# Performance work log

Measured on AMD Instinct MI355X. Metric: run time of the kernel, lower is better.

The kernel has to match this reference:

```python
import jax, jax.numpy as jnp
import numpy as np

B, C, H, W, L, R = 1, 32, 96, 128, 2, 3
N = 2 * R + 1
EPS = 1e-5


def conv2d(x, w, stride=1, pad=1):
    return jax.lax.conv_general_dilated(
        x, w, (stride, stride), ((pad, pad), (pad, pad)),
        dimension_numbers=('NCHW', 'OIHW', 'NCHW'))


def conv_transpose2d(x, w, stride=2, pad=1):
    # torch ConvTranspose2d semantics; w: [Cin, Cout, kH, kW]
    kh, kw = w.shape[2], w.shape[3]
    wf = jnp.flip(w, (2, 3)).transpose(1, 0, 2, 3)  # [Cout, Cin, kh, kw]
    return jax.lax.conv_general_dilated(
        x, wf, (1, 1),
        ((kh - 1 - pad, kh - 1 - pad), (kw - 1 - pad, kw - 1 - pad)),
        lhs_dilation=(stride, stride),
        dimension_numbers=('NCHW', 'OIHW', 'NCHW'))


def bnorm(x, s, b, m, v):
    # inference-mode BatchNorm2d (fixed running stats)
    inv = s * jax.lax.rsqrt(v + EPS)
    return x * inv[None, :, None, None] + (b - m * inv)[None, :, None, None]


def grid_sample(img, grid):
    # bilinear, align_corners=True, padding_mode='zeros'
    # img [B,C,H,W], grid [B,Hg,Wg,2] (x,y) in [-1,1]
    Bi, Ci, Hi, Wi = img.shape
    gx = (grid[..., 0] + 1.0) * 0.5 * (Wi - 1)
    gy = (grid[..., 1] + 1.0) * 0.5 * (Hi - 1)
    x0 = jnp.floor(gx)
    y0 = jnp.floor(gy)
    wx = (gx - x0)[:, None]  # [B,1,Hg,Wg]
    wy = (gy - y0)[:, None]

    def tap(yf, xf):
        valid = (xf >= 0) & (xf <= Wi - 1) & (yf >= 0) & (yf <= Hi - 1)
        xc = jnp.clip(xf, 0, Wi - 1).astype(jnp.int32)
        yc = jnp.clip(yf, 0, Hi - 1).astype(jnp.int32)
        v = jax.vmap(lambda im, y, x: im[:, y, x])(img, yc, xc)  # [B,C,Hg,Wg]
        return v * valid[:, None].astype(img.dtype)

    v00 = tap(y0, x0)
    v01 = tap(y0, x0 + 1)
    v10 = tap(y0 + 1, x0)
    v11 = tap(y0 + 1, x0 + 1)
    return (v00 * (1 - wx) * (1 - wy) + v01 * wx * (1 - wy)
            + v10 * (1 - wx) * wy + v11 * wx * wy)


def _forward(fmap1_0, fmap1_1, fmap2_0, fmap2_1, coords,
             cw1, cw2, cw3, cw4, ctw5, cw6, cb6,
             bn1s, bn1b, bn1m, bn1v, bn2s, bn2b, bn2m, bn2v,
             bn3s, bn3b, bn3m, bn3v, bn4s, bn4b, bn4m, bn4v,
             bn5s, bn5b, bn5m, bn5v, dap_w):
    n = N
    dx = jnp.linspace(-R, R, n)
    delta = jnp.stack(jnp.meshgrid(dx, dx, indexing='ij'), axis=-1)  # [n,n,2]
    b, _, h, w = coords.shape
    cp = coords.transpose(0, 2, 3, 1)  # [b,h,w,2] (x,y)
    bns = ((bn1s, bn1b, bn1m, bn1v), (bn2s, bn2b, bn2m, bn2v),
           (bn3s, bn3b, bn3m, bn3v), (bn4s, bn4b, bn4m, bn4v),
           (bn5s, bn5b, bn5m, bn5v))
    out = []
    for i, (f1, f2) in enumerate(((fmap1_0, fmap2_0), (fmap1_1, fmap2_1))):
        c, h2, w2 = f1.shape[1], f1.shape[2], f1.shape[3]
        # [b,n,h,n,w,2]: first n axis pairs with h, second with w (as in torch view)
        cent = cp[:, None, :, None, :, :] / (2.0 ** i) + delta[None, :, None, :, None, :]
        gx = 2.0 * cent[..., 0] / (w2 - 1) - 1.0
        gy = 2.0 * cent[..., 1] / (h2 - 1) - 1.0
        grid = jnp.stack([gx, gy], -1).reshape(b, n * h, n * w, 2)
        f2s = grid_sample(f2, grid).reshape(b, c, n, h, n, w)
        f2s = f2s.transpose(0, 2, 4, 1, 3, 5)  # [b,du,dv,c,h,w]
        f1e = jnp.broadcast_to(f1[:, None, None], (b, n, n, c, h, w))
        x = jnp.concatenate([f1e, f2s], axis=3).reshape(b * n * n, 2 * c, h, w)
        # MatchingNet (DICL): conv-bn-relu stack, stride-2 down + transposed up
        x = jax.nn.relu(bnorm(conv2d(x, cw1[i]), *(p[i] for p in bns[0])))
        x = jax.nn.relu(bnorm(conv2d(x, cw2[i], stride=2), *(p[i] for p in bns[1])))
        x = jax.nn.relu(bnorm(conv2d(x, cw3[i]), *(p[i] for p in bns[2])))
        x = jax.nn.relu(bnorm(conv2d(x, cw4[i]), *(p[i] for p in bns[3])))
        x = jax.nn.relu(bnorm(conv_transpose2d(x, ctw5[i]), *(p[i] for p in bns[4])))
        x = conv2d(x, cw6[i]) + cb6[i][None, :, None, None]  # [b*n*n,1,h,w]
        cost = x.reshape(b, n * n, h, w)
        # DisplacementAwareProjection: 1x1 conv over the 49 displacement channels
        cost = jnp.einsum('pq,bqhw->bphw', dap_w[i], cost)
        out.append(cost)
    return jnp.concatenate(out, axis=1)  # [b, L*(2r+1)^2, h, w]


def setup_inputs():
    key = jax.random.key(0)
    ks = jax.random.split(key, 40)

    def rn(k, shape, scale=1.0):
        return jax.random.normal(k, shape, jnp.float32) * scale

    inp = {}
    inp['fmap1_0'] = rn(ks[0], (B, C, H, W))
    inp['fmap2_0'] = rn(ks[1], (B, C, H, W))
    inp['fmap1_1'] = rn(ks[2], (B, C, H, W))
    inp['fmap2_1'] = rn(ks[3], (B, C, H, W))
    gy, gx = jnp.meshgrid(jnp.arange(H, dtype=jnp.float32),
                          jnp.arange(W, dtype=jnp.float32), indexing='ij')
    base = jnp.stack([gx, gy], 0)[None]  # [1,2,H,W] (x,y) pixel coords
    inp['coords'] = base + rn(ks[4], (B, 2, H, W), 2.0)

    def cw(k, co, ci, kk):
        return rn(k, (L, co, ci, kk, kk), 1.0 / np.sqrt(ci * kk * kk))

    inp['cw1'] = cw(ks[5], 96, 2 * C, 3)
    inp['cw2'] = cw(ks[6], 128, 96, 3)
    inp['cw3'] = cw(ks[7], 128, 128, 3)
    inp['cw4'] = cw(ks[8], 64, 128, 3)
    inp['ctw5'] = rn(ks[9], (L, 64, 32, 4, 4), 1.0 / np.sqrt(64 * 16))
    inp['cw6'] = cw(ks[10], 1, 32, 3)
    inp['cb6'] = rn(ks[11], (L, 1), 0.1)
    for j, ch in enumerate((96, 128, 128, 64, 32), start=1):
        k4 = jax.random.split(ks[11 + j], 4)
        inp['bn%ds' % j] = 1.0 + rn(k4[0], (L, ch), 0.1)
        inp['bn%db' % j] = rn(k4[1], (L, ch), 0.1)
        inp['bn%dm' % j] = rn(k4[2], (L, ch), 0.1)
        inp['bn%dv' % j] = 1.0 + rn(k4[3], (L, ch), 0.1) ** 2
    # DAP identity init
    inp['dap_w'] = jnp.tile(jnp.eye(N * N, dtype=jnp.float32)[None], (L, 1, 1))
    return inp


def reference(fmap1_0, fmap1_1, fmap2_0, fmap2_1, coords,
              cw1, cw2, cw3, cw4, ctw5, cw6, cb6,
              bn1s, bn1b, bn1m, bn1v, bn2s, bn2b, bn2m, bn2v,
              bn3s, bn3b, bn3m, bn3v, bn4s, bn4b, bn4m, bn4v,
              bn5s, bn5b, bn5m, bn5v, dap_w):
    return _forward(fmap1_0, fmap1_1, fmap2_0, fmap2_1, coords,
                    cw1, cw2, cw3, cw4, ctw5, cw6, cb6,
                    bn1s, bn1b, bn1m, bn1v, bn2s, bn2b, bn2m, bn2v,
                    bn3s, bn3b, bn3m, bn3v, bn4s, bn4b, bn4m, bn4v,
                    bn5s, bn5b, bn5m, bn5v, dap_w)
```

## Files before the change

kernel.cpp:

```cpp
#include <hip/hip_runtime.h>

#define EPSF 1e-5f

typedef __attribute__((ext_vector_type(8))) short short8;
typedef __attribute__((ext_vector_type(4))) float f32x4;

__device__ __forceinline__ ushort f2bf(float x) {
    union { float f; unsigned u; } c; c.f = x;
    unsigned r = c.u + 0x7FFF + ((c.u >> 16) & 1);
    return (ushort)(r >> 16);
}
__device__ __forceinline__ float bf2f(ushort b) {
    union { unsigned u; float f; } c; c.u = ((unsigned)b) << 16;
    return c.f;
}
__device__ __forceinline__ int swz(int a) {
    return a ^ (((a >> 7) & 7) << 4);
}


__global__ __launch_bounds__(256) void k_repack_conv(
    const float* __restrict__ src, ushort* __restrict__ dst, int CO, int CI)
{
    int idx = blockIdx.x * 256 + threadIdx.x;
    if (idx >= CO * CI * 9) return;
    int co = idx / (CI * 9);
    int rem = idx % (CI * 9);
    int ci = rem / 9, tap = rem % 9;
    dst[((size_t)tap * CO + co) * CI + ci] = f2bf(src[idx]);
}

__global__ __launch_bounds__(256) void k_repack_ct(
    const float* __restrict__ src, ushort* __restrict__ dst)
{
    int idx = blockIdx.x * 256 + threadIdx.x;
    if (idx >= 4 * 4 * 32 * 64) return;
    int ci = idx & 63;
    int t = idx >> 6;
    int co = t & 31; t >>= 5;
    int tap = t & 3;
    int parity = t >> 2;
    int ph = parity >> 1, pw = parity & 1;
    int a = tap >> 1, b = tap & 1;
    int kh = ((ph + 1) & 1) + 2 * a;
    int kw = ((pw + 1) & 1) + 2 * b;
    dst[idx] = f2bf(src[((ci * 32 + co) * 4 + kh) * 4 + kw]);
}

__global__ __launch_bounds__(256) void k_pack_f1(
    const float* __restrict__ f1_0, const float* __restrict__ f1_1,
    ushort* __restrict__ xf1)
{
    const int sp = blockIdx.x * 256 + threadIdx.x;
    const int l = blockIdx.z;
    const float* f1 = l ? f1_1 : f1_0;
    ushort* dst = xf1 + (size_t)l * 393216 + (size_t)sp * 32;
    #pragma unroll
    for (int g = 0; g < 4; ++g) {
        uint4 pk;
        uint* pw_ = (uint*)&pk;
        #pragma unroll
        for (int q = 0; q < 4; ++q) {
            int c = g * 8 + q * 2;
            pw_[q] = (uint)f2bf(f1[(size_t)c * 12288 + sp])
                   | ((uint)f2bf(f1[(size_t)(c + 1) * 12288 + sp]) << 16);
        }
        *(uint4*)(dst + g * 8) = pk;
    }
}

__global__ __launch_bounds__(256) void k_sample_nhwc(
    const float* __restrict__ f2_0, const float* __restrict__ f2_1,
    const float* __restrict__ coords, ushort* __restrict__ x0s, int d0)
{
    const int HW = 12288;
    const int sp = blockIdx.x * 256 + threadIdx.x;
    const int slot = blockIdx.z;
    const int p = d0 + slot;
    const int l = p / 49;
    const int d = p - l * 49;
    const int du = d / 7, dv = d % 7;
    const float inv_scale = l ? 0.5f : 1.0f;
    const float* f2 = l ? f2_1 : f2_0;

    float cx = coords[sp] * inv_scale + (float)(du - 3);
    float cy = coords[HW + sp] * inv_scale + (float)(dv - 3);
    float xf = floorf(cx), yf = floorf(cy);
    float wx = cx - xf, wy = cy - yf;
    int xi = (int)xf, yi = (int)yf;
    float vx0 = (xf >= 0.f && xf <= 127.f) ? 1.f : 0.f;
    float vx1 = (xf + 1.f >= 0.f && xf + 1.f <= 127.f) ? 1.f : 0.f;
    float vy0 = (yf >= 0.f && yf <= 95.f) ? 1.f : 0.f;
    float vy1 = (yf + 1.f >= 0.f && yf + 1.f <= 95.f) ? 1.f : 0.f;
    int x0i = min(max(xi, 0), 127), x1i = min(max(xi + 1, 0), 127);
    int y0i = min(max(yi, 0), 95),  y1i = min(max(yi + 1, 0), 95);
    float w00 = (1.f - wx) * (1.f - wy) * vx0 * vy0;
    float w01 = wx * (1.f - wy) * vx1 * vy0;
    float w10 = (1.f - wx) * wy * vx0 * vy1;
    float w11 = wx * wy * vx1 * vy1;
    int o00 = y0i * 128 + x0i, o01 = y0i * 128 + x1i;
    int o10 = y1i * 128 + x0i, o11 = y1i * 128 + x1i;

    ushort* dst = x0s + ((size_t)slot * HW + sp) * 32;
    #pragma unroll
    for (int g = 0; g < 4; ++g) {
        uint4 pk;
        uint* pw_ = (uint*)&pk;
        #pragma unroll
        for (int q = 0; q < 4; ++q) {
            uint wv = 0;
            #pragma unroll
            for (int h = 0; h < 2; ++h) {
                int c = g * 8 + q * 2 + h;
                const float* fc = f2 + (size_t)c * HW;
                float s = w00 * fc[o00] + w01 * fc[o01] + w10 * fc[o10] + w11 * fc[o11];
                wv |= ((uint)f2bf(s)) << (16 * h);
            }
            pw_[q] = wv;
        }
        *(uint4*)(dst + g * 8) = pk;
    }
}

template <int EPI>
__global__ __launch_bounds__(512, 2) void k_conv1(
    const ushort* __restrict__ in,
    ushort* __restrict__ out,
    const ushort* __restrict__ wbase,
    const float* __restrict__ p1,
    const float* __restrict__ bs0, const float* __restrict__ bb0,
    const float* __restrict__ bm0, const float* __restrict__ bv0,
    int d0, int koff)
{
    constexpr int AB = 10 * 66 * 64;
    constexpr int PB = 3 * 48 * 64;
    constexpr int SA = 6;
    __shared__ __align__(16) char smem[AB + 2 * PB];
    char* As = smem;

    const int tid = threadIdx.x;
    const int lane = tid & 63, wid = tid >> 6;
    const int lr = lane & 15, kg = lane >> 4;
    const int bx = blockIdx.x;
    const int rt = bx >> 1, ct = bx & 1;
    const int r0 = rt * 8, c0 = ct * 64;
    const int y = blockIdx.y;
    const int co0 = y * 48;
    const int slot = blockIdx.z;
    const int l = EPI ? slot : (d0 + slot) / 49;

    const ushort* ib = in + (size_t)slot * 12288 * 32;
    const ushort* wl = wbase + (size_t)l * (9 * 96 * 64);
    const short8 z8 = {0, 0, 0, 0, 0, 0, 0, 0};

    #pragma unroll
    for (int i = 0; i < SA; ++i) {
        int lin = i * 8192 + tid * 16;
        if (lin < AB) {
            int pos = lin >> 6;
            int prow = (pos * 994) >> 16;
            int pcol = pos - prow * 66;
            int grow = r0 - 1 + prow, gcol = c0 - 1 + pcol;
            bool ok = ((unsigned)grow < 96u) && ((unsigned)gcol < 128u);
            short8 v = z8;
            if (ok) v = *(const short8*)(ib + (grow * 128 + gcol) * 32 + ((lin & 63) >> 1));
            *(short8*)(As + swz(lin)) = v;
        }
    }

    int boff[2]; unsigned bmask = 0;
    #pragma unroll
    for (int i = 0; i < 2; ++i) {
        int lin = i * 8192 + tid * 16;
        if (lin < PB) bmask |= 1u << i;
        int lc = min(lin, PB - 16);
        int rowidx = lc >> 6;
        int tpg = rowidx / 48;
        int r = rowidx - tpg * 48;
        boff[i] = (tpg * 96 + co0 + r) * 64 + koff + ((lc & 63) >> 1);
    }
    short8 stgB[2];
    auto loadB = [&](int pg) {
        const ushort* src = wl + pg * (3 * 96 * 64);
        #pragma unroll
        for (int i = 0; i < 2; ++i)
            if ((bmask >> i) & 1) stgB[i] = *(const short8*)(src + boff[i]);
    };
    auto writeB = [&](int pg) {
        char* Bs = smem + AB + (pg & 1) * PB;
        #pragma unroll
        for (int i = 0; i < 2; ++i) {
            int lin = i * 8192 + tid * 16;
            if ((bmask >> i) & 1) *(short8*)(Bs + swz(lin)) = stgB[i];
        }
    };

    f32x4 acc[4][3];
    if constexpr (EPI == 0) {
        const float* pl = p1 + (size_t)l * 1179648
                        + ((size_t)((bx * 2 + y) * 512 + tid)) * 48;
        #pragma unroll
        for (int mf = 0; mf < 4; ++mf)
            #pragma unroll
            for (int nf = 0; nf < 3; ++nf)
                acc[mf][nf] = *(const f32x4*)(pl + (mf * 3 + nf) * 4);
    } else {
        #pragma unroll
        for (int mf = 0; mf < 4; ++mf)
            #pragma unroll
            for (int nf = 0; nf < 3; ++nf)
                acc[mf][nf] = (f32x4){0.f, 0.f, 0.f, 0.f};
    }

    loadB(0);
    writeB(0);
    __syncthreads();

    #pragma unroll
    for (int ps = 0; ps < 3; ++ps) {
        if (ps < 2) loadB(ps + 1);
        const char* Bs = smem + AB + (ps & 1) * PB;
        #pragma unroll
        for (int kw = 0; kw < 3; ++kw) {
            short8 a[4];
            #pragma unroll
            for (int mf = 0; mf < 4; ++mf) {
                int sp = (wid + ps) * 66 + mf * 16 + lr + kw;
                a[mf] = *(const short8*)(As + swz(sp * 64 + kg * 16));
            }
            #pragma unroll
            for (int nf = 0; nf < 3; ++nf) {
                short8 b = *(const short8*)(Bs + swz((kw * 48 + nf * 16 + lr) * 64 + kg * 16));
                #pragma unroll
                for (int mf = 0; mf < 4; ++mf)
                    acc[mf][nf] = __builtin_amdgcn_mfma_f32_16x16x32_bf16(
                        a[mf], b, acc[mf][nf], 0, 0, 0);
            }
        }
        __syncthreads();
        if (ps < 2) { writeB(ps + 1); __syncthreads(); }
    }

    if constexpr (EPI == 1) {
        float* of = (float*)out + (size_t)l * 1179648
                  + ((size_t)((bx * 2 + y) * 512 + tid)) * 48;
        #pragma unroll
        for (int mf = 0; mf < 4; ++mf)
            #pragma unroll
            for (int nf = 0; nf < 3; ++nf)
                *(f32x4*)(of + (mf * 3 + nf) * 4) = acc[mf][nf];
    } else {
        const float* bs = bs0 + l * 96;
        const float* bb = bb0 + l * 96;
        const float* bm = bm0 + l * 96;
        const float* bv = bv0 + l * 96;
        ushort* ob = out + (size_t)slot * 12288 * 96;
        const int orow = r0 + wid;
        #pragma unroll
        for (int nf = 0; nf < 3; ++nf) {
            const int col = co0 + nf * 16 + lr;
            const float inv = bs[col] * rsqrtf(bv[col] + EPSF);
            const float beta = bb[col] - bm[col] * inv;
            #pragma unroll
            for (int mf = 0; mf < 4; ++mf) {
                #pragma unroll
                for (int j = 0; j < 4; ++j) {
                    int ocol = c0 + mf * 16 + kg * 4 + j;
                    float yv = fmaxf(fmaf(acc[mf][nf][j], inv, beta), 0.f);
                    ob[((size_t)orow * 128 + ocol) * 96 + col] = f2bf(yv);
                }
            }
        }
    }
}

template <int CIN, int COUT, int IH, int IW>
__global__ __launch_bounds__(512, 4) void k_conv_lds8s(
    const ushort* __restrict__ in, ushort* __restrict__ out,
    const ushort* __restrict__ wbase, int wlstride,
    const float* __restrict__ bs0, const float* __restrict__ bb0,
    const float* __restrict__ bm0, const float* __restrict__ bv0, int d0)
{
    constexpr int CCs = CIN / 32;
    constexpr int AB = 10 * 66 * 64;
    constexpr int PB = 3 * 64 * 64;
    constexpr int SA = 6, SB = 2;
    constexpr int NPH = 3 * CCs;
    __shared__ __align__(16) char smem[AB + 2 * PB];
    char* As = smem;

    const int tid = threadIdx.x;
    const int lane = tid & 63, wid = tid >> 6;
    const int lr = lane & 15, kg = lane >> 4;
    const int r0 = (int)blockIdx.x * 8;
    const int co0 = (int)blockIdx.y * 64;
    const int slot = blockIdx.z;
    const int l = (d0 + slot) / 49;

    int aoff[SA]; unsigned awr = 0, avalid = 0;
    #pragma unroll
    for (int i = 0; i < SA; ++i) {
        int lin = i * 8192 + tid * 16;
        bool wr = lin < AB;
        int linc = wr ? lin : 0;
        int pos = linc >> 6;
        int prow = (pos * 994) >> 16;
        int pcol = pos - prow * 66;
        int grow = r0 - 1 + prow, gcol = pcol - 1;
        bool ok = wr && ((unsigned)grow < (unsigned)IH) && ((unsigned)gcol < (unsigned)IW);
        if (wr) awr |= 1u << i;
        if (ok) avalid |= 1u << i;
        int growc = min(max(grow, 0), IH - 1), gcolc = min(max(gcol, 0), IW - 1);
        aoff[i] = (growc * IW + gcolc) * CIN + ((linc & 63) >> 1);
    }
    int boff[SB]; unsigned bmask = 0;
    #pragma unroll
    for (int i = 0; i < SB; ++i) {
        int lin = i * 8192 + tid * 16;
        if (lin < PB) bmask |= 1u << i;
        int lc = min(lin, PB - 16);
        int rowidx = lc >> 6;
        int tpg = rowidx >> 6, r = rowidx & 63;
        boff[i] = (tpg * COUT + co0 + r) * CIN + ((lc & 63) >> 1);
    }

    const ushort* ib = in + (size_t)slot * IH * IW * CIN;
    const ushort* wl = wbase + (size_t)l * wlstride;
    const short8 z8 = {0, 0, 0, 0, 0, 0, 0, 0};

    auto stageA = [&](int cc) {
        #pragma unroll
        for (int i = 0; i < SA; ++i) {
            int lin = i * 8192 + tid * 16;
            if ((awr >> i) & 1) {
                short8 v = z8;
                if ((avalid >> i) & 1)
                    v = *(const short8*)(ib + aoff[i] + cc * 32);
                *(short8*)(As + swz(lin)) = v;
            }
        }
    };
    short8 stgB[SB];
    auto loadB = [&](int ps) {
        int pg = ps % 3, cc = ps / 3;
        const ushort* src = wl + pg * (3 * COUT * CIN) + cc * 32;
        #pragma unroll
        for (int i = 0; i < SB; ++i)
            if ((bmask >> i) & 1) stgB[i] = *(const short8*)(src + boff[i]);
    };
    auto writeB = [&](int ps) {
        char* Bs = smem + AB + (ps & 1) * PB;
        #pragma unroll
        for (int i = 0; i < SB; ++i) {
            int lin = i * 8192 + tid * 16;
            if ((bmask >> i) & 1) *(short8*)(Bs + swz(lin)) = stgB[i];
        }
    };

    f32x4 acc[4][4];
    #pragma unroll
    for (int mf = 0; mf < 4; ++mf)
        #pragma unroll
        for (int nf = 0; nf < 4; ++nf)
            acc[mf][nf] = (f32x4){0.f, 0.f, 0.f, 0.f};

    stageA(0);
    loadB(0); writeB(0);
    __syncthreads();

    #pragma unroll 1
    for (int ps = 0; ps < NPH; ++ps) {
        const int pg = ps % 3;
        const bool hasNext = (ps + 1 < NPH);
        if (hasNext) loadB(ps + 1);

        const char* Bs = smem + AB + (ps & 1) * PB;
        #pragma unroll
        for (int kw = 0; kw < 3; ++kw) {
            short8 a[4];
            #pragma unroll
            for (int mf = 0; mf < 4; ++mf) {
                int sp = (wid + pg) * 66 + mf * 16 + lr + kw;
                a[mf] = *(const short8*)(As + swz(sp * 64 + kg * 16));
            }
            #pragma unroll
            for (int nf = 0; nf < 4; ++nf) {
                short8 b = *(const short8*)(Bs + swz((kw * 64 + nf * 16 + lr) * 64 + kg * 16));
                #pragma unroll
                for (int mf = 0; mf < 4; ++mf)
                    acc[mf][nf] = __builtin_amdgcn_mfma_f32_16x16x32_bf16(
                        a[mf], b, acc[mf][nf], 0, 0, 0);
            }
        }

        __syncthreads();
        if (hasNext) {
            writeB(ps + 1);
            if (pg == 2) stageA(ps / 3 + 1);
            __syncthreads();
        }
    }

    const float* bs = bs0 + l * COUT;
    const float* bb = bb0 + l * COUT;
    const float* bm = bm0 + l * COUT;
    const float* bv = bv0 + l * COUT;
    ushort* ob = out + (size_t)slot * IH * IW * COUT;
    const int orow = r0 + wid;
    #pragma unroll
    for (int nf = 0; nf < 4; ++nf) {
        const int col = co0 + nf * 16 + lr;
        const float inv = bs[col] * rsqrtf(bv[col] + EPSF);
        const float beta = bb[col] - bm[col] * inv;
        #pragma unroll
        for (int mf = 0; mf < 4; ++mf) {
            #pragma unroll
            for (int j = 0; j < 4; ++j) {
                int ocol = mf * 16 + kg * 4 + j;
                float y = fmaxf(fmaf(acc[mf][nf][j], inv, beta), 0.f);
                ob[((size_t)orow * IW + ocol) * COUT + col] = f2bf(y);
            }
        }
    }
}

__global__ __launch_bounds__(512, 2) void k_conv_s2_8(
    const ushort* __restrict__ in, ushort* __restrict__ out,
    const ushort* __restrict__ wbase, int wlstride,
    const float* __restrict__ bs0, const float* __restrict__ bb0,
    const float* __restrict__ bm0, const float* __restrict__ bv0, int d0)
{
    constexpr int AB = 9 * 66 * 64;
    constexpr int PB = 3 * 64 * 64;
    constexpr int SA = 5;
    constexpr int SB = 2;
    constexpr int NPH = 9;
    __shared__ __align__(16) char smem[AB + 2 * PB];
    char* As = smem;

    const int tid = threadIdx.x;
    const int lane = tid & 63, wid = tid >> 6;
    const int lr = lane & 15, kg = lane >> 4;
    const int mw = wid >> 1, ch = wid & 1;
    const int bx = blockIdx.x;
    const int rt = bx >> 1, ct = bx & 1;
    const int r0 = rt * 4, oc0 = ct * 32;
    const int co0 = blockIdx.y * 64;
    const int slot = blockIdx.z;
    const int l = (d0 + slot) / 49;

    int aoff[SA]; unsigned awr = 0, avalid = 0;
    #pragma unroll
    for (int i = 0; i < SA; ++i) {
        int lin = i * 8192 + tid * 16;
        bool wr = lin < AB;
        int linc = wr ? lin : 0;
        int pos = linc >> 6;
        int prow = (pos * 994) >> 16;
        int pcol = pos - prow * 66;
        int grow = 2 * r0 - 1 + prow, gcol = 2 * oc0 - 1 + pcol;
        bool ok = wr && ((unsigned)grow < 96u) && ((unsigned)gcol < 128u);
        if (wr) awr |= 1u << i;
        if (ok) avalid |= 1u << i;
        int growc = min(max(grow, 0), 95), gcolc = min(max(gcol, 0), 127);
        aoff[i] = (growc * 128 + gcolc) * 96 + ((linc & 63) >> 1);
    }
    int boff[SB]; unsigned bmask = 0;
    #pragma unroll
    for (int i = 0; i < SB; ++i) {
        int lin = i * 8192 + tid * 16;
        if (lin < PB) bmask |= 1u << i;
        int lc = min(lin, PB - 16);
        int rowidx = lc >> 6;
        int tpg = rowidx >> 6, r = rowidx & 63;
        boff[i] = (tpg * 128 + co0 + r) * 96 + ((lc & 63) >> 1);
    }

    const ushort* ib = in + (size_t)slot * 12288 * 96;
    const ushort* wl = wbase + (size_t)l * wlstride;
    const short8 z8 = {0, 0, 0, 0, 0, 0, 0, 0};

    short8 stgA[SA], stgB[SB];
    auto loadA = [&](int cc) {
        #pragma unroll
        for (int i = 0; i < SA; ++i) {
            if ((avalid >> i) & 1) stgA[i] = *(const short8*)(ib + aoff[i] + cc * 32);
            else stgA[i] = z8;
        }
    };
    auto writeA = [&]() {
        #pragma unroll
        for (int i = 0; i < SA; ++i) {
            int lin = i * 8192 + tid * 16;
            if ((awr >> i) & 1)
                *(short8*)(As + swz(lin)) = stgA[i];
        }
    };
    auto loadB = [&](int ps) {
        int pg = ps % 3, cc = ps / 3;
        const ushort* src = wl + pg * (3 * 128 * 96) + cc * 32;
        #pragma unroll
        for (int i = 0; i < SB; ++i)
            if ((bmask >> i) & 1) stgB[i] = *(const short8*)(src + boff[i]);
    };
    auto writeB = [&](int ps) {
        char* Bs = smem + AB + (ps & 1) * PB;
        #pragma unroll
        for (int i = 0; i < SB; ++i) {
            int lin = i * 8192 + tid * 16;
            if ((bmask >> i) & 1)
                *(short8*)(Bs + swz(lin)) = stgB[i];
        }
    };

    f32x4 acc[2][2];
    #pragma unroll
    for (int mf = 0; mf < 2; ++mf)
        #pragma unroll
        for (int nf = 0; nf < 2; ++nf)
            acc[mf][nf] = (f32x4){0.f, 0.f, 0.f, 0.f};

    loadA(0); loadB(0);
    writeA(); writeB(0);
    __syncthreads();

    #pragma unroll 1
    for (int ps = 0; ps < NPH; ++ps) {
        const int pg = ps % 3;
        const bool hasNext = (ps + 1 < NPH);
        const bool newA = (pg == 2) && hasNext;
        if (hasNext) loadB(ps + 1);
        if (newA) loadA(ps / 3 + 1);

        const char* Bs = smem + AB + (ps & 1) * PB;
        #pragma unroll
        for (int kw = 0; kw < 3; ++kw) {
            short8 a[2];
            #pragma unroll
            for (int mf = 0; mf < 2; ++mf) {
                int pos = (2 * mw + pg) * 66 + 2 * (mf * 16 + lr) + kw;
                a[mf] = *(const short8*)(As + swz(pos * 64 + kg * 16));
            }
            #pragma unroll
            for (int nf = 0; nf < 2; ++nf) {
                int rb = kw * 64 + ch * 32 + nf * 16 + lr;
                short8 b = *(const short8*)(Bs + swz(rb * 64 + kg * 16));
                #pragma unroll
                for (int mf = 0; mf < 2; ++mf)
                    acc[mf][nf] = __builtin_amdgcn_mfma_f32_16x16x32_bf16(
                        a[mf], b, acc[mf][nf], 0, 0, 0);
            }
        }

        __syncthreads();
        if (hasNext) writeB(ps + 1);
        if (newA) writeA();
        if (hasNext) __syncthreads();
    }

    const float* bs = bs0 + l * 128;
    const float* bb = bb0 + l * 128;
    const float* bm = bm0 + l * 128;
    const float* bv = bv0 + l * 128;
    ushort* ob = out + (size_t)slot * 3072 * 128;
    const int orow = r0 + mw;
    #pragma unroll
    for (int nf = 0; nf < 2; ++nf) {
        const int col = co0 + ch * 32 + nf * 16 + lr;
        const float inv = bs[col] * rsqrtf(bv[col] + EPSF);
        const float beta = bb[col] - bm[col] * inv;
        #pragma unroll
        for (int mf = 0; mf < 2; ++mf) {
            #pragma unroll
            for (int j = 0; j < 4; ++j) {
                int ocol = oc0 + mf * 16 + kg * 4 + j;
                float y = fmaxf(fmaf(acc[mf][nf][j], inv, beta), 0.f);
                ob[((size_t)orow * 64 + ocol) * 128 + col] = f2bf(y);
            }
        }
    }
}

__global__ __launch_bounds__(512, 4) void k_convt_lds(
    const ushort* __restrict__ in, ushort* __restrict__ out,
    const ushort* __restrict__ wbase,
    const float* __restrict__ bs0, const float* __restrict__ bb0,
    const float* __restrict__ bm0, const float* __restrict__ bv0, int d0)
{
    constexpr int AB = 10 * 66 * 64;
    constexpr int PB = 4 * 32 * 64;
    constexpr int SA = 6;
    __shared__ __align__(16) char smem[AB + 2 * PB];
    char* As = smem;

    const int tid = threadIdx.x;
    const int lane = tid & 63, wid = tid >> 6;
    const int lr = lane & 15, kg = lane >> 4;
    const int q0 = (int)blockIdx.x * 8;
    const int parity = blockIdx.y;
    const int ph = parity >> 1, pw = parity & 1;
    const int slot = blockIdx.z;
    const int l = (d0 + slot) / 49;

    int aoff[SA]; unsigned awr = 0, avalid = 0;
    #pragma unroll
    for (int i = 0; i < SA; ++i) {
        int lin = i * 8192 + tid * 16;
        bool wr = lin < AB;
        int linc = wr ? lin : 0;
        int pos = linc >> 6;
        int prow = (pos * 994) >> 16;
        int pcol = pos - prow * 66;
        int grow = q0 - 1 + prow, gcol = pcol - 1;
        bool ok = wr && ((unsigned)grow < 48u) && ((unsigned)gcol < 64u);
        if (wr) awr |= 1u << i;
        if (ok) avalid |= 1u << i;
        int growc = min(max(grow, 0), 47), gcolc = min(max(gcol, 0), 63);
        aoff[i] = (growc * 64 + gcolc) * 64 + ((linc & 63) >> 1);
    }
    int boffB;
    {
        int lin = tid * 16;
        int rowidx = lin >> 6;
        int tap = rowidx >> 5, co = rowidx & 31;
        boffB = ((parity * 4 + tap) * 32 + co) * 64 + ((lin & 63) >> 1);
    }

    const ushort* ib = in + (size_t)slot * 3072 * 64;
    const ushort* wl = wbase + (size_t)l * (16 * 32 * 64);
    const short8 z8 = {0, 0, 0, 0, 0, 0, 0, 0};

    auto stageA = [&](int cc) {
        #pragma unroll
        for (int i = 0; i < SA; ++i) {
            int lin = i * 8192 + tid * 16;
            if ((awr >> i) & 1) {
                short8 v = z8;
                if ((avalid >> i) & 1)
                    v = *(const short8*)(ib + aoff[i] + cc * 32);
                *(short8*)(As + swz(lin)) = v;
            }
        }
    };
    short8 stgB;
    auto loadB = [&](int cc) {
        stgB = *(const short8*)(wl + boffB + cc * 32);
    };
    auto writeB = [&](int cc) {
        char* Bs = smem + AB + (cc & 1) * PB;
        *(short8*)(Bs + swz(tid * 16)) = stgB;
    };

    f32x4 acc[4][2];
    #pragma unroll
    for (int mf = 0; mf < 4; ++mf)
        #pragma unroll
        for (int nf = 0; nf < 2; ++nf)
            acc[mf][nf] = (f32x4){0.f, 0.f, 0.f, 0.f};

    stageA(0);
    loadB(0); writeB(0);
    __syncthreads();

    #pragma unroll 1
    for (int cc = 0; cc < 2; ++cc) {
        if (cc == 0) loadB(1);
        const char* Bs = smem + AB + (cc & 1) * PB;
        #pragma unroll
        for (int a = 0; a < 2; ++a) {
            #pragma unroll
            for (int b2 = 0; b2 < 2; ++b2) {
                const int tap = a * 2 + b2;
                short8 av[4];
                #pragma unroll
                for (int mf = 0; mf < 4; ++mf) {
                    int pos = (wid + 1 + ph - a) * 66 + mf * 16 + lr + pw - b2 + 1;
                    av[mf] = *(const short8*)(As + swz(pos * 64 + kg * 16));
                }
                #pragma unroll
                for (int nf = 0; nf < 2; ++nf) {
                    short8 b = *(const short8*)(Bs
                        + swz((tap * 32 + nf * 16 + lr) * 64 + kg * 16));
                    #pragma unroll
                    for (int mf = 0; mf < 4; ++mf)
                        acc[mf][nf] = __builtin_amdgcn_mfma_f32_16x16x32_bf16(
                            av[mf], b, acc[mf][nf], 0, 0, 0);
                }
            }
        }
        __syncthreads();
        if (cc == 0) {
            writeB(1);
            stageA(1);
            __syncthreads();
        }
    }

    const float* bs = bs0 + l * 32;
    const float* bb = bb0 + l * 32;
    const float* bm = bm0 + l * 32;
    const float* bv = bv0 + l * 32;
    ushort* ob = out + (size_t)slot * 12288 * 32;
    const size_t rowb = (size_t)(2 * (q0 + wid) + ph) * 128;
    #pragma unroll
    for (int nf = 0; nf < 2; ++nf) {
        const int col = nf * 16 + lr;
        const float inv = bs[col] * rsqrtf(bv[col] + EPSF);
        const float beta = bb[col] - bm[col] * inv;
        #pragma unroll
        for (int mf = 0; mf < 4; ++mf) {
            #pragma unroll
            for (int j = 0; j < 4; ++j) {
                int r = mf * 16 + kg * 4 + j;
                float y = fmaxf(fmaf(acc[mf][nf][j], inv, beta), 0.f);
                ob[(rowb + 2 * r + pw) * 32 + col] = f2bf(y);
            }
        }
    }
}

__global__ __launch_bounds__(256) void k_conv6(
    const ushort* __restrict__ x5, float* __restrict__ cost,
    const float* __restrict__ w0, const float* __restrict__ cb6, int d0)
{
    const int sp = blockIdx.x * 256 + threadIdx.x;
    const int slot = blockIdx.z;
    const int p = d0 + slot;
    const int l = p / 49;
    const float* w = w0 + l * 288;
    const int oh = sp >> 7, ow = sp & 127;
    float acc = 0.f;
    #pragma unroll
    for (int kh = 0; kh < 3; ++kh) {
        const int ih = oh - 1 + kh;
        if (ih < 0 || ih >= 96) continue;
        #pragma unroll
        for (int kw = 0; kw < 3; ++kw) {
            const int iw = ow - 1 + kw;
            if (iw < 0 || iw >= 128) continue;
            const ushort* q = x5 + ((size_t)slot * 12288 + ih * 128 + iw) * 32;
            const int tap = kh * 3 + kw;
            #pragma unroll
            for (int g = 0; g < 4; ++g) {
                uint4 v = *(const uint4*)(q + g * 8);
                const uint* vw = (const uint*)&v;
                #pragma unroll
                for (int t = 0; t < 4; ++t) {
                    int ci = g * 8 + t * 2;
                    acc = fmaf(bf2f((ushort)(vw[t] & 0xFFFF)), w[ci * 9 + tap], acc);
                    acc = fmaf(bf2f((ushort)(vw[t] >> 16)), w[(ci + 1) * 9 + tap], acc);
                }
            }
        }
    }
    cost[(size_t)p * 12288 + sp] = acc + cb6[l];
}

__global__ __launch_bounds__(256) void k_dap(
    const float* __restrict__ cost, const float* __restrict__ dw,
    float* __restrict__ out)
{
    const int sp = blockIdx.x * 256 + threadIdx.x;
    const int p = blockIdx.y;
    const float* dr = dw + p * 49;
    float acc = 0.f;
    #pragma unroll
    for (int q = 0; q < 49; ++q)
        acc = fmaf(dr[q], cost[(size_t)q * 12288 + sp], acc);
    out[(size_t)p * 12288 + sp] = acc;
}

extern "C" void kernel_launch(void* const* d_in, const int* in_sizes, int n_in,
                              void* d_out, int out_size, void* d_ws, size_t ws_size,
                              hipStream_t stream)
{
    const float* fm1_0 = (const float*)d_in[0];
    const float* fm2_0 = (const float*)d_in[1];
    const float* fm1_1 = (const float*)d_in[2];
    const float* fm2_1 = (const float*)d_in[3];
    const float* coords = (const float*)d_in[4];
    const float* cw1  = (const float*)d_in[5];
    const float* cw2  = (const float*)d_in[6];
    const float* cw3  = (const float*)d_in[7];
    const float* cw4  = (const float*)d_in[8];
    const float* ctw5 = (const float*)d_in[9];
    const float* cw6  = (const float*)d_in[10];
    const float* cb6  = (const float*)d_in[11];
    const float* bn[5][4];
    for (int j = 0; j < 5; ++j)
        for (int k = 0; k < 4; ++k)
            bn[j][k] = (const float*)d_in[12 + j * 4 + k];
    const float* dap = (const float*)d_in[32];
    float* out = (float*)d_out;

    const size_t A_US = 393216;
    const size_t B_US = 1179648;
    const size_t XF1 = 2 * 393216;
    const size_t W1 = 9 * 96 * 64, W2 = 9 * 128 * 96, W3 = 9 * 128 * 128;
    const size_t W4 = 9 * 64 * 128, W5 = 16 * 32 * 64;
    const size_t W_US = 2 * (W1 + W2 + W3 + W4 + W5);
    const size_t P1F = 2 * (size_t)24 * 2 * 512 * 48;
    const size_t COSTF = (size_t)98 * 12288;

    int DC = 1;
    for (int cand : {98, 66, 49, 42, 33, 25, 17, 13, 9, 7, 5, 3, 2, 1}) {
        size_t need = (A_US + B_US) * (size_t)cand * 2 + (XF1 + W_US) * 2
                    + (P1F + COSTF) * 4 + 4096;
        if (need <= ws_size) { DC = cand; break; }
    }

    ushort* bufA = (ushort*)d_ws;
    ushort* bufB = bufA + A_US * DC;
    ushort* xf1 = bufB + B_US * DC;
    ushort* wp = xf1 + XF1;
    ushort* wr1 = wp; wp += 2 * W1;
    ushort* wr2 = wp; wp += 2 * W2;
    ushort* wr3 = wp; wp += 2 * W3;
    ushort* wr4 = wp; wp += 2 * W4;
    ushort* wr5 = wp; wp += 2 * W5;
    float* P1 = (float*)wp;
    float* cost = P1 + P1F;

    for (int l = 0; l < 2; ++l) {
        k_repack_conv<<<dim3(216), 256, 0, stream>>>(cw1 + (size_t)l * W1, wr1 + l * W1, 96, 64);
        k_repack_conv<<<dim3(432), 256, 0, stream>>>(cw2 + (size_t)l * W2, wr2 + l * W2, 128, 96);
        k_repack_conv<<<dim3(576), 256, 0, stream>>>(cw3 + (size_t)l * W3, wr3 + l * W3, 128, 128);
        k_repack_conv<<<dim3(288), 256, 0, stream>>>(cw4 + (size_t)l * W4, wr4 + l * W4, 64, 128);
        k_repack_ct<<<dim3(128), 256, 0, stream>>>(ctw5 + (size_t)l * W5, wr5 + l * W5);
    }

    k_pack_f1<<<dim3(48, 1, 2), 256, 0, stream>>>(fm1_0, fm1_1, xf1);
    k_conv1<1><<<dim3(24, 2, 2), 512, 0, stream>>>(
        xf1, (ushort*)P1, wr1, nullptr,
        bn[0][0], bn[0][1], bn[0][2], bn[0][3], 0, 0);

    for (int d0 = 0; d0 < 98; d0 += DC) {
        const int ndd = min(DC, 98 - d0);
        k_sample_nhwc<<<dim3(48, 1, ndd), 256, 0, stream>>>(
            fm2_0, fm2_1, coords, bufA, d0);
        k_conv1<0><<<dim3(24, 2, ndd), 512, 0, stream>>>(
            bufA, bufB, wr1, P1,
            bn[0][0], bn[0][1], bn[0][2], bn[0][3], d0, 32);
        k_conv_s2_8<<<dim3(24, 2, ndd), 512, 0, stream>>>(bufB, bufA, wr2, (int)W2,
                bn[1][0], bn[1][1], bn[1][2], bn[1][3], d0);
        k_conv_lds8s<128, 128, 48, 64>
            <<<dim3(6, 2, ndd), 512, 0, stream>>>(bufA, bufB, wr3, (int)W3,
                bn[2][0], bn[2][1], bn[2][2], bn[2][3], d0);
        k_conv_lds8s<128, 64, 48, 64>
            <<<dim3(6, 1, ndd), 512, 0, stream>>>(bufB, bufA, wr4, (int)W4,
                bn[3][0], bn[3][1], bn[3][2], bn[3][3], d0);
        k_convt_lds<<<dim3(6, 4, ndd), 512, 0, stream>>>(bufA, bufB, wr5,
                bn[4][0], bn[4][1], bn[4][2], bn[4][3], d0);
        k_conv6<<<dim3(48, 1, ndd), 256, 0, stream>>>(
            bufB, cost, cw6, cb6, d0);
    }
    for (int l = 0; l < 2; ++l)
        k_dap<<<dim3(48, 49), 256, 0, stream>>>(
            cost + (size_t)l * 49 * 12288, dap + (size_t)l * 49 * 49,
            out + (size_t)l * 49 * 12288);
}
```

Baseline: 735.8 us.

## Compute all 128 output channels per block in stride-2 conv, single-buffer weights

```diff
diff --git a/kernel.cpp b/kernel.cpp
--- a/kernel.cpp
+++ b/kernel.cpp
@@ -424,28 +424,28 @@
     }
 }
 
-__global__ __launch_bounds__(512, 2) void k_conv_s2_8(
+__global__ __launch_bounds__(512, 4) void k_conv_s2_8(
     const ushort* __restrict__ in, ushort* __restrict__ out,
     const ushort* __restrict__ wbase, int wlstride,
     const float* __restrict__ bs0, const float* __restrict__ bb0,
     const float* __restrict__ bm0, const float* __restrict__ bv0, int d0)
 {
     constexpr int AB = 9 * 66 * 64;
-    constexpr int PB = 3 * 64 * 64;
+    constexpr int PB = 3 * 128 * 64;
     constexpr int SA = 5;
-    constexpr int SB = 2;
+    constexpr int SB = 3;
     constexpr int NPH = 9;
-    __shared__ __align__(16) char smem[AB + 2 * PB];
+    __shared__ __align__(16) char smem[AB + PB];
     char* As = smem;
 
     const int tid = threadIdx.x;
     const int lane = tid & 63, wid = tid >> 6;
     const int lr = lane & 15, kg = lane >> 4;
-    const int mw = wid >> 1, ch = wid & 1;
+    const int mw = wid >> 2;
+    const int cw = wid & 3;
     const int bx = blockIdx.x;
     const int rt = bx >> 1, ct = bx & 1;
     const int r0 = rt * 4, oc0 = ct * 32;
-    const int co0 = blockIdx.y * 64;
     const int slot = blockIdx.z;
     const int l = (d0 + slot) / 49;
 
@@ -465,97 +465,92 @@
         int growc = min(max(grow, 0), 95), gcolc = min(max(gcol, 0), 127);
         aoff[i] = (growc * 128 + gcolc) * 96 + ((linc & 63) >> 1);
     }
-    int boff[SB]; unsigned bmask = 0;
+    int boff[SB];
     #pragma unroll
     for (int i = 0; i < SB; ++i) {
         int lin = i * 8192 + tid * 16;
-        if (lin < PB) bmask |= 1u << i;
-        int lc = min(lin, PB - 16);
-        int rowidx = lc >> 6;
-        int tpg = rowidx >> 6, r = rowidx & 63;
-        boff[i] = (tpg * 128 + co0 + r) * 96 + ((lc & 63) >> 1);
+        int rowidx = lin >> 6;
+        int tpg = rowidx >> 7, r = rowidx & 127;
+        boff[i] = (tpg * 128 + r) * 96 + ((lin & 63) >> 1);
     }
 
     const ushort* ib = in + (size_t)slot * 12288 * 96;
     const ushort* wl = wbase + (size_t)l * wlstride;
     const short8 z8 = {0, 0, 0, 0, 0, 0, 0, 0};
 
-    short8 stgA[SA], stgB[SB];
-    auto loadA = [&](int cc) {
-        #pragma unroll
-        for (int i = 0; i < SA; ++i) {
-            if ((avalid >> i) & 1) stgA[i] = *(const short8*)(ib + aoff[i] + cc * 32);
-            else stgA[i] = z8;
-        }
-    };
-    auto writeA = [&]() {
+    auto stageA = [&](int cc) {
         #pragma unroll
         for (int i = 0; i < SA; ++i) {
             int lin = i * 8192 + tid * 16;
-            if ((awr >> i) & 1)
-                *(short8*)(As + swz(lin)) = stgA[i];
-        }
-    };
+            if ((awr >> i) & 1) {
+                short8 v = z8;
+                if ((avalid >> i) & 1)
+                    v = *(const short8*)(ib + aoff[i] + cc * 32);
+                *(short8*)(As + swz(lin)) = v;
+            }
+        }
+    };
+    short8 stgB[SB];
     auto loadB = [&](int ps) {
         int pg = ps % 3, cc = ps / 3;
         const ushort* src = wl + pg * (3 * 128 * 96) + cc * 32;
         #pragma unroll
         for (int i = 0; i < SB; ++i)
-            if ((bmask >> i) & 1) stgB[i] = *(const short8*)(src + boff[i]);
-    };
-    auto writeB = [&](int ps) {
-        char* Bs = smem + AB + (ps & 1) * PB;
+            stgB[i] = *(const short8*)(src + boff[i]);
+    };
+    auto writeB = [&]() {
+        char* Bs = smem + AB;
         #pragma unroll
         for (int i = 0; i < SB; ++i) {
             int lin = i * 8192 + tid * 16;
-            if ((bmask >> i) & 1)
-                *(short8*)(Bs + swz(lin)) = stgB[i];
-        }
-    };
-
-    f32x4 acc[2][2];
-    #pragma unroll
-    for (int mf = 0; mf < 2; ++mf)
+            *(short8*)(Bs + swz(lin)) = stgB[i];
+        }
+    };
+
+    f32x4 acc[4][2];
+    #pragma unroll
+    for (int mf = 0; mf < 4; ++mf)
         #pragma unroll
         for (int nf = 0; nf < 2; ++nf)
             acc[mf][nf] = (f32x4){0.f, 0.f, 0.f, 0.f};
 
-    loadA(0); loadB(0);
-    writeA(); writeB(0);
+    stageA(0);
+    loadB(0); writeB();
     __syncthreads();
 
     #pragma unroll 1
     for (int ps = 0; ps < NPH; ++ps) {
         const int pg = ps % 3;
         const bool hasNext = (ps + 1 < NPH);
-        const bool newA = (pg == 2) && hasNext;
         if (hasNext) loadB(ps + 1);
-        if (newA) loadA(ps / 3 + 1);
-
-        const char* Bs = smem + AB + (ps & 1) * PB;
+
+        const char* Bs = smem + AB;
         #pragma unroll
         for (int kw = 0; kw < 3; ++kw) {
-            short8 a[2];
-            #pragma unroll
-            for (int mf = 0; mf < 2; ++mf) {
-                int pos = (2 * mw + pg) * 66 + 2 * (mf * 16 + lr) + kw;
+            short8 a[4];
+            #pragma unroll
+            for (int mf = 0; mf < 4; ++mf) {
+                int pos = (2 * (mw * 2 + (mf >> 1)) + pg) * 66
+                        + 2 * ((mf & 1) * 16 + lr) + kw;
                 a[mf] = *(const short8*)(As + swz(pos * 64 + kg * 16));
             }
             #pragma unroll
             for (int nf = 0; nf < 2; ++nf) {
-                int rb = kw * 64 + ch * 32 + nf * 16 + lr;
+                int rb = kw * 128 + cw * 32 + nf * 16 + lr;
                 short8 b = *(const short8*)(Bs + swz(rb * 64 + kg * 16));
                 #pragma unroll
-                for (int mf = 0; mf < 2; ++mf)
+                for (int mf = 0; mf < 4; ++mf)
                     acc[mf][nf] = __builtin_amdgcn_mfma_f32_16x16x32_bf16(
                         a[mf], b, acc[mf][nf], 0, 0, 0);
             }
         }
 
         __syncthreads();
-        if (hasNext) writeB(ps + 1);
-        if (newA) writeA();
-        if (hasNext) __syncthreads();
+        if (hasNext) {
+            writeB();
+            if (pg == 2) stageA(ps / 3 + 1);
+            __syncthreads();
+        }
     }
 
     const float* bs = bs0 + l * 128;
@@ -563,17 +558,17 @@
     const float* bm = bm0 + l * 128;
     const float* bv = bv0 + l * 128;
     ushort* ob = out + (size_t)slot * 3072 * 128;
-    const int orow = r0 + mw;
     #pragma unroll
     for (int nf = 0; nf < 2; ++nf) {
-        const int col = co0 + ch * 32 + nf * 16 + lr;
+        const int col = cw * 32 + nf * 16 + lr;
         const float inv = bs[col] * rsqrtf(bv[col] + EPSF);
         const float beta = bb[col] - bm[col] * inv;
         #pragma unroll
-        for (int mf = 0; mf < 2; ++mf) {
+        for (int mf = 0; mf < 4; ++mf) {
+            const int orow = r0 + mw * 2 + (mf >> 1);
             #pragma unroll
             for (int j = 0; j < 4; ++j) {
-                int ocol = oc0 + mf * 16 + kg * 4 + j;
+                int ocol = oc0 + (mf & 1) * 16 + kg * 4 + j;
                 float y = fmaxf(fmaf(acc[mf][nf][j], inv, beta), 0.f);
                 ob[((size_t)orow * 64 + ocol) * 128 + col] = f2bf(y);
             }
@@ -841,7 +836,7 @@
         k_conv1<0><<<dim3(24, 2, ndd), 512, 0, stream>>>(
             bufA, bufB, wr1, P1,
             bn[0][0], bn[0][1], bn[0][2], bn[0][3], d0, 32);
-        k_conv_s2_8<<<dim3(24, 2, ndd), 512, 0, stream>>>(bufB, bufA, wr2, (int)W2,
+        k_conv_s2_8<<<dim3(24, 1, ndd), 512, 0, stream>>>(bufB, bufA, wr2, (int)W2,
                 bn[1][0], bn[1][1], bn[1][2], bn[1][3], d0);
         k_conv_lds8s<128, 128, 48, 64>
             <<<dim3(6, 2, ndd), 512, 0, stream>>>(bufA, bufB, wr3, (int)W3,
```

After: 734.4 us. About the same (-0.2%).
